# Optimization experiments

Measured on AMD Instinct MI355X. Metric: run time of the kernel, lower is better.

Reference implementation:

```python
import jax, jax.numpy as jnp
import numpy as np

LN2 = 0.69314718  # matches the 2ln2 constant in the original rbf()


def setup_inputs() -> dict:
    key = jax.random.key(0)
    domain_min = [-1.0, -1.0, -1.0]
    domain_max = [1.0, 1.0, 1.0]
    n = [12, 12, 12]
    codomain_dim = 128
    N = 200000

    axes = [jnp.linspace(domain_min[i], domain_max[i], n[i], dtype=jnp.float32)
            for i in range(len(n))]
    # torch.meshgrid default is 'ij' indexing
    grid = jnp.stack(jnp.meshgrid(*axes, indexing='ij'), axis=-1).reshape(-1, len(n))  # [G, 3]

    # rbf_width: mean nearest-neighbor distance on the grid (second-smallest per row)
    d = jnp.linalg.norm(grid[:, None, :] - grid[None, :, :], axis=-1)  # [G, G], G=1728 -> small
    width = jnp.sort(d, axis=1)[:, 1].mean()

    # interpolation matrix m and coeffs = solve(m, weight), as in __init__ (no_grad buffer)
    m = jnp.exp(-(d ** 2) / (width ** 2 / LN2))
    k1, k2 = jax.random.split(key)
    weight = jax.random.normal(k1, (grid.shape[0], codomain_dim), dtype=jnp.float32)
    coeffs = jnp.linalg.solve(m, weight)  # [G, C]

    x = jax.random.normal(k2, (N, len(n)), dtype=jnp.float32)  # [N, 3]
    return {"x": x, "grid": grid, "coeffs": coeffs, "width": width}


def reference(x, grid, coeffs, width):
    # Squared Euclidean distance via |a|^2 + |b|^2 - 2ab (avoids [N, G, 3] broadcast tensor).
    # rbf(d, w) = exp(-d^2 / (w^2 / ln2)); since it only uses d^2, skip the sqrt.
    x2 = jnp.sum(x * x, axis=-1, keepdims=True)          # [N, 1]
    g2 = jnp.sum(grid * grid, axis=-1)                   # [G]
    d2 = x2 + g2[None, :] - 2.0 * (x @ grid.T)           # [N, G]
    d2 = jnp.maximum(d2, 0.0)                            # numerical guard
    p = jnp.exp(-d2 * (LN2 / (width * width)))           # [N, G]
    return p @ coeffs                                    # [N, C]
```

## Files before the change

### kernel.cpp

```cpp
#include <hip/hip_runtime.h>
#include <stdint.h>


typedef _Float16 f16;
typedef _Float16 f16x8 __attribute__((ext_vector_type(8)));
typedef float f32x16 __attribute__((ext_vector_type(16)));

#define LN2F 0.69314718f
#define LOG2E 1.4426950408889634f

#define CD 128
#define KD 1728

__global__ void prep_coeffs(const float* __restrict__ coeffs,
                            f16* __restrict__ img) {
  int kp  = blockIdx.x * 2 + (threadIdx.x >> 7);
  int col = threadIdx.x & 127;
  int i   = kp / 144;
  int r   = kp - i * 144;
  int s   = r >> 4;
  int idx = r & 15;
  int hh  = idx >> 3;
  int b   = idx & 7;
  int j, k2;
  if (s < 6) { j = 2 * s + hh;                 k2 = b; }
  else       { j = 4 * (s - 6) + 2 * hh + (b >> 2); k2 = 8 + (b & 3); }
  float v = coeffs[(size_t)((i * 12 + j) * 12 + k2) * CD + col];
  f16 h = (f16)v;
  f16 l = (f16)(v - (float)h);
  int q   = i * 9 + s;
  int ch2 = col >> 6;
  int c64 = col & 63;
  size_t o = (size_t)q * 4096 + ch2 * 2048 + hh * 512 + c64 * 8 + b;
  img[o]        = h;
  img[o + 1024] = l;
}

union FU { uint32_t u[4]; f16x8 v; };

__global__ __launch_bounds__(128) void rbf_gemm(
    const float* __restrict__ x,
    const float* __restrict__ width,
    const f16* __restrict__ img,
    float* __restrict__ out, int N) {
  const int t    = threadIdx.x;
  const int lane = t & 63;
  const int wv   = t >> 6;
  const int l31  = lane & 31;
  const int hh   = lane >> 5;
  const int rbase = blockIdx.x * 128;
  const int ch2   = blockIdx.y;

  const float w  = width[0];
  const float s2 = (LN2F * LOG2E) / (w * w);

  int r0 = rbase + wv * 64 + l31;      if (r0 >= N) r0 = N - 1;
  int r1 = rbase + wv * 64 + 32 + l31; if (r1 >= N) r1 = N - 1;
  const float x00 = x[(size_t)r0 * 3 + 0];
  const float x01 = x[(size_t)r0 * 3 + 1];
  const float x02 = x[(size_t)r0 * 3 + 2];
  const float x10 = x[(size_t)r1 * 3 + 0];
  const float x11 = x[(size_t)r1 * 3 + 1];
  const float x12 = x[(size_t)r1 * 3 + 2];

  float e1a[2][12], e2a[2][12];
#pragma unroll
  for (int k = 0; k < 12; ++k) {
    float g = (float)k * (2.0f / 11.0f) - 1.0f;
    float d;
    d = x01 - g; e1a[0][k] = __builtin_amdgcn_exp2f(-d * d * s2);
    d = x11 - g; e1a[1][k] = __builtin_amdgcn_exp2f(-d * d * s2);
    d = x02 - g; e2a[0][k] = __builtin_amdgcn_exp2f(-d * d * s2);
    d = x12 - g; e2a[1][k] = __builtin_amdgcn_exp2f(-d * d * s2);
  }

  const int voff = ch2 * 4096 + hh * 1024 + l31 * 16;
  const char* imgb = (const char*)img;

  f16x8 cb0 = *(const f16x8*)(imgb + voff + 0);
  f16x8 cb1 = *(const f16x8*)(imgb + voff + 512);
  f16x8 cb2 = *(const f16x8*)(imgb + voff + 2048);
  f16x8 cb3 = *(const f16x8*)(imgb + voff + 2560);
  f16x8 db0 = *(const f16x8*)(imgb + 8192 + voff + 0);
  f16x8 db1 = *(const f16x8*)(imgb + 8192 + voff + 512);
  f16x8 db2 = *(const f16x8*)(imgb + 8192 + voff + 2048);
  f16x8 db3 = *(const f16x8*)(imgb + 8192 + voff + 2560);

  f32x16 acc00, acc01, acc10, acc11;
#pragma unroll
  for (int q = 0; q < 16; ++q) { acc00[q] = 0.f; acc01[q] = 0.f; acc10[q] = 0.f; acc11[q] = 0.f; }

#pragma unroll 1
  for (int i = 0; i < 12; ++i) {
    float gi = (float)i * (2.0f / 11.0f) - 1.0f;
    float d0;
    d0 = x00 - gi; float e00 = __builtin_amdgcn_exp2f(-d0 * d0 * s2);
    d0 = x10 - gi; float e01v = __builtin_amdgcn_exp2f(-d0 * d0 * s2);

#pragma unroll
    for (int s = 0; s < 9; ++s) {
      const char* spn = imgb + (size_t)(i * 9 + s + 2) * 8192;
      f16x8 nb0 = *(const f16x8*)(spn + voff + 0);
      f16x8 nb1 = *(const f16x8*)(spn + voff + 512);
      f16x8 nb2 = *(const f16x8*)(spn + voff + 2048);
      f16x8 nb3 = *(const f16x8*)(spn + voff + 2560);

      FU ah0, al0, ah1, al1;
#pragma unroll
      for (int mi = 0; mi < 2; ++mi) {
        float e0i = mi ? e01v : e00;
        FU* pah = mi ? &ah1 : &ah0;
        FU* pal = mi ? &al1 : &al0;
        if (s < 6) {
          float es = e0i * (hh ? e1a[mi][2 * s + 1] : e1a[mi][2 * s]);
#pragma unroll
          for (int q = 0; q < 4; ++q) {
            float ea = e2a[mi][2 * q];
            float eb = e2a[mi][2 * q + 1];
            uint32_t hq, lq;
            asm("v_fma_mixlo_f16 %0, %1, %2, 0"
                : "=v"(hq) : "v"(es), "v"(ea));
            asm("v_fma_mixhi_f16 %0, %1, %2, 0"
                : "+v"(hq) : "v"(es), "v"(eb));
            asm("v_fma_mixlo_f16 %0, %1, %2, -%3 op_sel:[0,0,0] op_sel_hi:[0,0,1]"
                : "=v"(lq) : "v"(es), "v"(ea), "v"(hq));
            asm("v_fma_mixhi_f16 %0, %1, %2, -%3 op_sel:[0,0,1] op_sel_hi:[0,0,1]"
                : "+v"(lq) : "v"(es), "v"(eb), "v"(hq));
            pah->u[q] = hq;
            pal->u[q] = lq;
          }
        } else {
          int J0 = 4 * (s - 6);
          float c01 = e0i * (hh ? e1a[mi][J0 + 2] : e1a[mi][J0 + 0]);
          float c23 = e0i * (hh ? e1a[mi][J0 + 3] : e1a[mi][J0 + 1]);
#pragma unroll
          for (int q = 0; q < 4; ++q) {
            float es = (q < 2) ? c01 : c23;
            float ea = e2a[mi][8 + 2 * (q & 1)];
            float eb = e2a[mi][9 + 2 * (q & 1)];
            uint32_t hq, lq;
            asm("v_fma_mixlo_f16 %0, %1, %2, 0"
                : "=v"(hq) : "v"(es), "v"(ea));
            asm("v_fma_mixhi_f16 %0, %1, %2, 0"
                : "+v"(hq) : "v"(es), "v"(eb));
            asm("v_fma_mixlo_f16 %0, %1, %2, -%3 op_sel:[0,0,0] op_sel_hi:[0,0,1]"
                : "=v"(lq) : "v"(es), "v"(ea), "v"(hq));
            asm("v_fma_mixhi_f16 %0, %1, %2, -%3 op_sel:[0,0,1] op_sel_hi:[0,0,1]"
                : "+v"(lq) : "v"(es), "v"(eb), "v"(hq));
            pah->u[q] = hq;
            pal->u[q] = lq;
          }
        }
      }

      __builtin_amdgcn_s_setprio(1);
      acc00 = __builtin_amdgcn_mfma_f32_32x32x16_f16(ah0.v, cb0, acc00, 0, 0, 0);
      acc01 = __builtin_amdgcn_mfma_f32_32x32x16_f16(ah0.v, cb1, acc01, 0, 0, 0);
      acc10 = __builtin_amdgcn_mfma_f32_32x32x16_f16(ah1.v, cb0, acc10, 0, 0, 0);
      acc11 = __builtin_amdgcn_mfma_f32_32x32x16_f16(ah1.v, cb1, acc11, 0, 0, 0);
      acc00 = __builtin_amdgcn_mfma_f32_32x32x16_f16(al0.v, cb0, acc00, 0, 0, 0);
      acc01 = __builtin_amdgcn_mfma_f32_32x32x16_f16(al0.v, cb1, acc01, 0, 0, 0);
      acc10 = __builtin_amdgcn_mfma_f32_32x32x16_f16(al1.v, cb0, acc10, 0, 0, 0);
      acc11 = __builtin_amdgcn_mfma_f32_32x32x16_f16(al1.v, cb1, acc11, 0, 0, 0);
      acc00 = __builtin_amdgcn_mfma_f32_32x32x16_f16(ah0.v, cb2, acc00, 0, 0, 0);
      acc01 = __builtin_amdgcn_mfma_f32_32x32x16_f16(ah0.v, cb3, acc01, 0, 0, 0);
      acc10 = __builtin_amdgcn_mfma_f32_32x32x16_f16(ah1.v, cb2, acc10, 0, 0, 0);
      acc11 = __builtin_amdgcn_mfma_f32_32x32x16_f16(ah1.v, cb3, acc11, 0, 0, 0);
      __builtin_amdgcn_s_setprio(0);

      cb0 = db0; cb1 = db1; cb2 = db2; cb3 = db3;
      db0 = nb0; db1 = nb1; db2 = nb2; db3 = nb3;
    }
  }

#pragma unroll
  for (int q = 0; q < 16; ++q) {
    int row0 = rbase + wv * 64 + (q & 3) + 8 * (q >> 2) + 4 * hh;
    int col  = ch2 * 64 + l31;
    if (row0 < N) {
      out[(size_t)row0 * CD + col]      = acc00[q];
      out[(size_t)row0 * CD + col + 32] = acc01[q];
    }
    int row1 = row0 + 32;
    if (row1 < N) {
      out[(size_t)row1 * CD + col]      = acc10[q];
      out[(size_t)row1 * CD + col + 32] = acc11[q];
    }
  }
}

__global__ void rbf_fallback(const float* __restrict__ x, const float* __restrict__ grid,
                             const float* __restrict__ coeffs, const float* __restrict__ width,
                             float* __restrict__ out, int N) {
  int row = blockIdx.x;
  int col = threadIdx.x;
  if (row >= N) return;
  float x0 = x[(size_t)row * 3 + 0];
  float x1 = x[(size_t)row * 3 + 1];
  float x2 = x[(size_t)row * 3 + 2];
  float w = width[0];
  float s2 = (LN2F * LOG2E) / (w * w);
  float acc = 0.f;
  for (int g = 0; g < 1728; ++g) {
    float d0 = x0 - grid[g * 3 + 0];
    float d1 = x1 - grid[g * 3 + 1];
    float d2 = x2 - grid[g * 3 + 2];
    float p = exp2f(-(d0 * d0 + d1 * d1 + d2 * d2) * s2);
    acc += p * coeffs[(size_t)g * CD + col];
  }
  out[(size_t)row * CD + col] = acc;
}

extern "C" void kernel_launch(void* const* d_in, const int* in_sizes, int n_in,
                              void* d_out, int out_size, void* d_ws, size_t ws_size,
                              hipStream_t stream) {
  const float* x      = (const float*)d_in[0];
  const float* grid   = (const float*)d_in[1];
  const float* coeffs = (const float*)d_in[2];
  const float* width  = (const float*)d_in[3];
  float* out = (float*)d_out;
  int N = in_sizes[0] / 3;

  size_t need = (size_t)108 * 8192 + 2 * 8192;
  if (ws_size >= need) {
    f16* img = (f16*)d_ws;
    hipLaunchKernelGGL(prep_coeffs, dim3(KD / 2), dim3(256), 0, stream,
                       coeffs, img);
    int nb = (N + 127) / 128;
    hipLaunchKernelGGL(rbf_gemm, dim3(nb, 2), dim3(128), 0, stream,
                       x, width, img, out, N);
  } else {
    hipLaunchKernelGGL(rbf_fallback, dim3(N), dim3(CD), 0, stream,
                       x, grid, coeffs, width, out, N);
  }
}
```

Before: 246.1 us.

## Interleave hi/lo A-fragment conversion with MFMA groups and triple-buffer B loads

Splits the per-step A-operand construction so the high fp16 parts are built first and fed to MFMAs while the low residual parts are computed afterwards, interleaving VALU work with matrix-core issue. Replaces the two-deep B-fragment register rotation with a three-slot ring, issuing the next loads between MFMA groups. The aim is better overlap of conversion ALU work, global loads and MFMA execution. It may raise register pressure and relies on the compiler resolving the ring indices statically after unrolling.

```diff
diff --git a/kernel.cpp b/kernel.cpp
--- a/kernel.cpp
+++ b/kernel.cpp
@@ -77,14 +77,13 @@
   const int voff = ch2 * 4096 + hh * 1024 + l31 * 16;
   const char* imgb = (const char*)img;
 
-  f16x8 cb0 = *(const f16x8*)(imgb + voff + 0);
-  f16x8 cb1 = *(const f16x8*)(imgb + voff + 512);
-  f16x8 cb2 = *(const f16x8*)(imgb + voff + 2048);
-  f16x8 cb3 = *(const f16x8*)(imgb + voff + 2560);
-  f16x8 db0 = *(const f16x8*)(imgb + 8192 + voff + 0);
-  f16x8 db1 = *(const f16x8*)(imgb + 8192 + voff + 512);
-  f16x8 db2 = *(const f16x8*)(imgb + 8192 + voff + 2048);
-  f16x8 db3 = *(const f16x8*)(imgb + 8192 + voff + 2560);
+  f16x8 B0[4], B1[4], B2[4];
+#pragma unroll
+  for (int f = 0; f < 4; ++f) {
+    const int off = (f & 1) * 512 + (f >> 1) * 2048;
+    B0[f] = *(const f16x8*)(imgb + voff + off);
+    B1[f] = *(const f16x8*)(imgb + 8192 + voff + off);
+  }
 
   f32x16 acc00, acc01, acc10, acc11;
 #pragma unroll
@@ -99,77 +98,100 @@
 
 #pragma unroll
     for (int s = 0; s < 9; ++s) {
-      const char* spn = imgb + (size_t)(i * 9 + s + 2) * 8192;
-      f16x8 nb0 = *(const f16x8*)(spn + voff + 0);
-      f16x8 nb1 = *(const f16x8*)(spn + voff + 512);
-      f16x8 nb2 = *(const f16x8*)(spn + voff + 2048);
-      f16x8 nb3 = *(const f16x8*)(spn + voff + 2560);
+      f16x8* CUR = (s % 3 == 0) ? B0 : (s % 3 == 1) ? B1 : B2;
+      f16x8* NXT = (s % 3 == 0) ? B2 : (s % 3 == 1) ? B0 : B1;
+
+      float es0, es1, c010, c230, c011, c231;
+      if (s < 6) {
+        es0 = e00  * (hh ? e1a[0][2 * s + 1] : e1a[0][2 * s]);
+        es1 = e01v * (hh ? e1a[1][2 * s + 1] : e1a[1][2 * s]);
+      } else {
+        int J0 = 4 * (s - 6);
+        c010 = e00  * (hh ? e1a[0][J0 + 2] : e1a[0][J0 + 0]);
+        c230 = e00  * (hh ? e1a[0][J0 + 3] : e1a[0][J0 + 1]);
+        c011 = e01v * (hh ? e1a[1][J0 + 2] : e1a[1][J0 + 0]);
+        c231 = e01v * (hh ? e1a[1][J0 + 3] : e1a[1][J0 + 1]);
+      }
 
       FU ah0, al0, ah1, al1;
 #pragma unroll
-      for (int mi = 0; mi < 2; ++mi) {
-        float e0i = mi ? e01v : e00;
-        FU* pah = mi ? &ah1 : &ah0;
-        FU* pal = mi ? &al1 : &al0;
+      for (int q = 0; q < 4; ++q) {
+        float ea0, eb0, ea1, eb1, esa0, esa1;
         if (s < 6) {
-          float es = e0i * (hh ? e1a[mi][2 * s + 1] : e1a[mi][2 * s]);
-#pragma unroll
-          for (int q = 0; q < 4; ++q) {
-            float ea = e2a[mi][2 * q];
-            float eb = e2a[mi][2 * q + 1];
-            uint32_t hq, lq;
-            asm("v_fma_mixlo_f16 %0, %1, %2, 0"
-                : "=v"(hq) : "v"(es), "v"(ea));
-            asm("v_fma_mixhi_f16 %0, %1, %2, 0"
-                : "+v"(hq) : "v"(es), "v"(eb));
-            asm("v_fma_mixlo_f16 %0, %1, %2, -%3 op_sel:[0,0,0] op_sel_hi:[0,0,1]"
-                : "=v"(lq) : "v"(es), "v"(ea), "v"(hq));
-            asm("v_fma_mixhi_f16 %0, %1, %2, -%3 op_sel:[0,0,1] op_sel_hi:[0,0,1]"
-                : "+v"(lq) : "v"(es), "v"(eb), "v"(hq));
-            pah->u[q] = hq;
-            pal->u[q] = lq;
-          }
+          ea0 = e2a[0][2 * q];     eb0 = e2a[0][2 * q + 1];
+          ea1 = e2a[1][2 * q];     eb1 = e2a[1][2 * q + 1];
+          esa0 = es0; esa1 = es1;
         } else {
-          int J0 = 4 * (s - 6);
-          float c01 = e0i * (hh ? e1a[mi][J0 + 2] : e1a[mi][J0 + 0]);
-          float c23 = e0i * (hh ? e1a[mi][J0 + 3] : e1a[mi][J0 + 1]);
-#pragma unroll
-          for (int q = 0; q < 4; ++q) {
-            float es = (q < 2) ? c01 : c23;
-            float ea = e2a[mi][8 + 2 * (q & 1)];
-            float eb = e2a[mi][9 + 2 * (q & 1)];
-            uint32_t hq, lq;
-            asm("v_fma_mixlo_f16 %0, %1, %2, 0"
-                : "=v"(hq) : "v"(es), "v"(ea));
-            asm("v_fma_mixhi_f16 %0, %1, %2, 0"
-                : "+v"(hq) : "v"(es), "v"(eb));
-            asm("v_fma_mixlo_f16 %0, %1, %2, -%3 op_sel:[0,0,0] op_sel_hi:[0,0,1]"
-                : "=v"(lq) : "v"(es), "v"(ea), "v"(hq));
-            asm("v_fma_mixhi_f16 %0, %1, %2, -%3 op_sel:[0,0,1] op_sel_hi:[0,0,1]"
-                : "+v"(lq) : "v"(es), "v"(eb), "v"(hq));
-            pah->u[q] = hq;
-            pal->u[q] = lq;
-          }
+          ea0 = e2a[0][8 + 2 * (q & 1)];  eb0 = e2a[0][9 + 2 * (q & 1)];
+          ea1 = e2a[1][8 + 2 * (q & 1)];  eb1 = e2a[1][9 + 2 * (q & 1)];
+          esa0 = (q < 2) ? c010 : c230;
+          esa1 = (q < 2) ? c011 : c231;
         }
+        uint32_t h0, h1;
+        asm("v_fma_mixlo_f16 %0, %1, %2, 0" : "=v"(h0) : "v"(esa0), "v"(ea0));
+        asm("v_fma_mixhi_f16 %0, %1, %2, 0" : "+v"(h0) : "v"(esa0), "v"(eb0));
+        asm("v_fma_mixlo_f16 %0, %1, %2, 0" : "=v"(h1) : "v"(esa1), "v"(ea1));
+        asm("v_fma_mixhi_f16 %0, %1, %2, 0" : "+v"(h1) : "v"(esa1), "v"(eb1));
+        ah0.u[q] = h0;
+        ah1.u[q] = h1;
       }
 
       __builtin_amdgcn_s_setprio(1);
-      acc00 = __builtin_amdgcn_mfma_f32_32x32x16_f16(ah0.v, cb0, acc00, 0, 0, 0);
-      acc01 = __builtin_amdgcn_mfma_f32_32x32x16_f16(ah0.v, cb1, acc01, 0, 0, 0);
-      acc10 = __builtin_amdgcn_mfma_f32_32x32x16_f16(ah1.v, cb0, acc10, 0, 0, 0);
-      acc11 = __builtin_amdgcn_mfma_f32_32x32x16_f16(ah1.v, cb1, acc11, 0, 0, 0);
-      acc00 = __builtin_amdgcn_mfma_f32_32x32x16_f16(al0.v, cb0, acc00, 0, 0, 0);
-      acc01 = __builtin_amdgcn_mfma_f32_32x32x16_f16(al0.v, cb1, acc01, 0, 0, 0);
-      acc10 = __builtin_amdgcn_mfma_f32_32x32x16_f16(al1.v, cb0, acc10, 0, 0, 0);
-      acc11 = __builtin_amdgcn_mfma_f32_32x32x16_f16(al1.v, cb1, acc11, 0, 0, 0);
-      acc00 = __builtin_amdgcn_mfma_f32_32x32x16_f16(ah0.v, cb2, acc00, 0, 0, 0);
-      acc01 = __builtin_amdgcn_mfma_f32_32x32x16_f16(ah0.v, cb3, acc01, 0, 0, 0);
-      acc10 = __builtin_amdgcn_mfma_f32_32x32x16_f16(ah1.v, cb2, acc10, 0, 0, 0);
-      acc11 = __builtin_amdgcn_mfma_f32_32x32x16_f16(ah1.v, cb3, acc11, 0, 0, 0);
+      acc00 = __builtin_amdgcn_mfma_f32_32x32x16_f16(ah0.v, CUR[0], acc00, 0, 0, 0);
+      acc01 = __builtin_amdgcn_mfma_f32_32x32x16_f16(ah0.v, CUR[1], acc01, 0, 0, 0);
+      acc10 = __builtin_amdgcn_mfma_f32_32x32x16_f16(ah1.v, CUR[0], acc10, 0, 0, 0);
+      acc11 = __builtin_amdgcn_mfma_f32_32x32x16_f16(ah1.v, CUR[1], acc11, 0, 0, 0);
       __builtin_amdgcn_s_setprio(0);
 
-      cb0 = db0; cb1 = db1; cb2 = db2; cb3 = db3;
-      db0 = nb0; db1 = nb1; db2 = nb2; db3 = nb3;
+#pragma unroll
+      for (int q = 0; q < 4; ++q) {
+        float ea0, eb0, ea1, eb1, esa0, esa1;
+        if (s < 6) {
+          ea0 = e2a[0][2 * q];     eb0 = e2a[0][2 * q + 1];
+          ea1 = e2a[1][2 * q];     eb1 = e2a[1][2 * q + 1];
+          esa0 = es0; esa1 = es1;
+        } else {
+          ea0 = e2a[0][8 + 2 * (q & 1)];  eb0 = e2a[0][9 + 2 * (q & 1)];
+          ea1 = e2a[1][8 + 2 * (q & 1)];  eb1 = e2a[1][9 + 2 * (q & 1)];
+          esa0 = (q < 2) ? c010 : c230;
+          esa1 = (q < 2) ? c011 : c231;
+        }
+        uint32_t l0, l1;
+        uint32_t h0 = ah0.u[q], h1 = ah1.u[q];
+        asm("v_fma_mixlo_f16 %0, %1, %2, -%3 op_sel:[0,0,0] op_sel_hi:[0,0,1]"
+            : "=v"(l0) : "v"(esa0), "v"(ea0), "v"(h0));
+        asm("v_fma_mixhi_f16 %0, %1, %2, -%3 op_sel:[0,0,1] op_sel_hi:[0,0,1]"
+            : "+v"(l0) : "v"(esa0), "v"(eb0), "v"(h0));
+        asm("v_fma_mixlo_f16 %0, %1, %2, -%3 op_sel:[0,0,0] op_sel_hi:[0,0,1]"
+            : "=v"(l1) : "v"(esa1), "v"(ea1), "v"(h1));
+        asm("v_fma_mixhi_f16 %0, %1, %2, -%3 op_sel:[0,0,1] op_sel_hi:[0,0,1]"
+            : "+v"(l1) : "v"(esa1), "v"(eb1), "v"(h1));
+        al0.u[q] = l0;
+        al1.u[q] = l1;
+      }
+
+      __builtin_amdgcn_s_setprio(1);
+      acc00 = __builtin_amdgcn_mfma_f32_32x32x16_f16(al0.v, CUR[0], acc00, 0, 0, 0);
+      acc01 = __builtin_amdgcn_mfma_f32_32x32x16_f16(al0.v, CUR[1], acc01, 0, 0, 0);
+      acc10 = __builtin_amdgcn_mfma_f32_32x32x16_f16(al1.v, CUR[0], acc10, 0, 0, 0);
+      acc11 = __builtin_amdgcn_mfma_f32_32x32x16_f16(al1.v, CUR[1], acc11, 0, 0, 0);
+      __builtin_amdgcn_s_setprio(0);
+
+      {
+        const char* spn = imgb + (size_t)(i * 9 + s + 2) * 8192;
+#pragma unroll
+        for (int f = 0; f < 4; ++f) {
+          const int off = (f & 1) * 512 + (f >> 1) * 2048;
+          NXT[f] = *(const f16x8*)(spn + voff + off);
+        }
+      }
+
+      __builtin_amdgcn_s_setprio(1);
+      acc00 = __builtin_amdgcn_mfma_f32_32x32x16_f16(ah0.v, CUR[2], acc00, 0, 0, 0);
+      acc01 = __builtin_amdgcn_mfma_f32_32x32x16_f16(ah0.v, CUR[3], acc01, 0, 0, 0);
+      acc10 = __builtin_amdgcn_mfma_f32_32x32x16_f16(ah1.v, CUR[2], acc10, 0, 0, 0);
+      acc11 = __builtin_amdgcn_mfma_f32_32x32x16_f16(ah1.v, CUR[3], acc11, 0, 0, 0);
+      __builtin_amdgcn_s_setprio(0);
     }
   }
 
```

Measured after the change: 246.7 us. About the same (+0.3%).
